# Optimization experiments

Hardware: AMD Instinct MI355X
Metric: run time of the kernel (lower is better)

The kernel has to match this reference:

```python
import jax, jax.numpy as jnp
import numpy as np
import math

B, T, C, H = 4, 2048, 768, 12
HS = C // H  # 64


def setup_inputs() -> dict:
    key = jax.random.key(0)
    ks = jax.random.split(key, 6)
    s = 1.0 / math.sqrt(C)
    return {
        "x": jax.random.normal(ks[0], (B, T, C), dtype=jnp.float32),
        "memory": jax.random.normal(ks[1], (B, T, C), dtype=jnp.float32),
        "Wq": jax.random.normal(ks[2], (C, C), dtype=jnp.float32) * s,
        "bq": jnp.zeros((C,), dtype=jnp.float32),
        "Wkv": jax.random.normal(ks[3], (C, 2 * C), dtype=jnp.float32) * s,
        "bkv": jnp.zeros((2 * C,), dtype=jnp.float32),
        "Wproj": jax.random.normal(ks[4], (C, C), dtype=jnp.float32) * s,
        "bproj": jnp.zeros((C,), dtype=jnp.float32),
    }


def reference(x, memory, Wq, bq, Wkv, bkv, Wproj, bproj):
    # q projection of decoder stream x, kv projection of encoder memory
    q = x @ Wq + bq                      # [B,T,C]
    kv = memory @ Wkv + bkv              # [B,T,2C]
    k, v = jnp.split(kv, 2, axis=2)      # [B,T,C] each

    def heads(t):
        return t.reshape(B, T, H, HS).transpose(0, 2, 1, 3)  # [B,H,T,hs]

    q, k, v = heads(q), heads(k), heads(v)
    scale = 1.0 / math.sqrt(HS)
    att = jnp.einsum("bhqd,bhkd->bhqk", q, k) * scale        # [B,H,T,T]
    att = jax.nn.softmax(att, axis=-1)
    y = jnp.einsum("bhqk,bhkd->bhqd", att, v)                # [B,H,T,hs]
    y = y.transpose(0, 2, 1, 3).reshape(B, T, C)
    return y @ Wproj + bproj
```

## Files before the change

kernel.cpp:

```cpp
#include <hip/hip_runtime.h>
#include <hip/hip_bf16.h>


#define B_  4
#define T_  2048
#define C_  768
#define H_  12
#define HS_ 64

typedef __attribute__((ext_vector_type(8))) short short8;
typedef __attribute__((ext_vector_type(4))) float f32x4;

__device__ __forceinline__ short f2bf(float f) {
    __hip_bfloat16 h = __float2bfloat16(f);
    return *reinterpret_cast<short*>(&h);
}

__device__ __forceinline__ void gload_lds16(const void* g, void* l) {
    __builtin_amdgcn_global_load_lds((const __attribute__((address_space(1))) void*)g,
                                     (__attribute__((address_space(3))) void*)l,
                                     16, 0, 0);
}


__global__ void prepass(const float* __restrict__ x, short* __restrict__ xb,
                        const float* __restrict__ mem, short* __restrict__ memb,
                        const float* __restrict__ Wq,  short* __restrict__ WqT,
                        const float* __restrict__ Wkv, short* __restrict__ WkvT,
                        const float* __restrict__ Wp,  short* __restrict__ WpT,
                        float qscale) {
    const int n4 = 8192 * 768 / 4;
    const int cvtblocks = (2 * n4) / 256;
    int bid = blockIdx.x;
    if (bid < cvtblocks) {
        int i = bid * 256 + threadIdx.x;
        const float* in; short* out;
        if (i < n4) { in = x; out = xb; }
        else        { in = mem; out = memb; i -= n4; }
        float4 v = reinterpret_cast<const float4*>(in)[i];
        short4 o;
        o.x = f2bf(v.x); o.y = f2bf(v.y); o.z = f2bf(v.z); o.w = f2bf(v.w);
        reinterpret_cast<short4*>(out)[i] = o;
        return;
    }
    __shared__ float tile[32][33];
    bid -= cvtblocks;
    const float* in; short* out; int N; float sc = 1.0f;
    if (bid < 576)       { in = Wq;  out = WqT;  N = 768;  sc = qscale; }
    else if (bid < 1728) { in = Wkv; out = WkvT; N = 1536; bid -= 576; }
    else                 { in = Wp;  out = WpT;  N = 768;  bid -= 1728; }
    const int tiles_n = N >> 5;
    const int k0 = (bid / tiles_n) * 32;
    const int n0 = (bid % tiles_n) * 32;
    const int r = threadIdx.x >> 5;
    const int c = threadIdx.x & 31;
    #pragma unroll
    for (int i = 0; i < 4; ++i)
        tile[r + 8 * i][c] = in[(size_t)(k0 + r + 8 * i) * N + n0 + c];
    __syncthreads();
    #pragma unroll
    for (int i = 0; i < 4; ++i)
        out[(size_t)(n0 + r + 8 * i) * 768 + k0 + c] = f2bf(tile[c][r + 8 * i] * sc);
}


template<int OUT_F32, int WRITE_VT>
__device__ __forceinline__ void gemm_body(const short* __restrict__ A, const short* __restrict__ BT,
                                          const float* __restrict__ bias, void* __restrict__ out,
                                          short* __restrict__ vt,
                                          int m0, int n0, int K, int ldo, float bscale,
                                          short (*As)[64], short (*Bs)[64]) {
    const int t  = threadIdx.x;
    const int wid = t >> 6;
    const int wm = wid >> 1, wn = wid & 1;
    const int lane = t & 63;
    const int lr = lane & 15;
    const int lk = (lane >> 4) * 8;

    f32x4 acc[4][4] = {};

    const int srow = wid * 32 + (lane >> 3);
    const int scol = (lane & 7) * 8;

    for (int k0 = 0; k0 < K; k0 += 64) {
        __syncthreads();
        #pragma unroll
        for (int i = 0; i < 4; ++i)
            gload_lds16(&A[(size_t)(m0 + srow + i * 8) * K + k0 + scol],
                        &As[wid * 32 + i * 8][0]);
        #pragma unroll
        for (int i = 0; i < 4; ++i)
            gload_lds16(&BT[(size_t)(n0 + srow + i * 8) * K + k0 + scol],
                        &Bs[wid * 32 + i * 8][0]);
        __syncthreads();

        #pragma unroll
        for (int ks = 0; ks < 2; ++ks) {
            const int kk = ks * 32 + lk;
            short8 a[4], b[4];
            #pragma unroll
            for (int m = 0; m < 4; ++m)
                a[m] = *reinterpret_cast<const short8*>(&As[wm*64 + m*16 + lr][kk]);
            #pragma unroll
            for (int n = 0; n < 4; ++n)
                b[n] = *reinterpret_cast<const short8*>(&Bs[wn*64 + n*16 + lr][kk]);
            #pragma unroll
            for (int m = 0; m < 4; ++m)
                #pragma unroll
                for (int n = 0; n < 4; ++n)
                    acc[m][n] = __builtin_amdgcn_mfma_f32_16x16x32_bf16(a[m], b[n], acc[m][n], 0, 0, 0);
        }
    }

    const int rb = m0 + wm * 64;
    const int cb = n0 + wn * 64;
    const int rj = (lane >> 4) * 4;
    #pragma unroll
    for (int n = 0; n < 4; ++n) {
        const int col = cb + n * 16 + lr;
        const float bv = bias[col] * bscale;
        #pragma unroll
        for (int m = 0; m < 4; ++m) {
            #pragma unroll
            for (int j = 0; j < 4; ++j) {
                const int row = rb + m * 16 + rj + j;
                const float v = acc[m][n][j] + bv;
                if (WRITE_VT && col >= 768) {
                    const int vd = col - 768;
                    const int hh = vd >> 6, dd = vd & 63;
                    const int bb = row >> 11, tt = row & 2047;
                    const int kv = tt & 63;
                    const int slot = 32 * (kv >> 5) + 8 * ((kv >> 2) & 3)
                                   + 4 * ((kv >> 4) & 1) + (kv & 3);
                    const int ptt = (tt & ~63) | slot;
                    vt[(((size_t)bb * H_ + hh) * HS_ + dd) * T_ + ptt] = f2bf(v);
                } else if (OUT_F32) {
                    reinterpret_cast<float*>(out)[(size_t)row * ldo + col] = v;
                } else {
                    reinterpret_cast<short*>(out)[(size_t)row * ldo + col] = f2bf(v);
                }
            }
        }
    }
}

__global__ void gemm_qkv(const short* __restrict__ xb,  const short* __restrict__ memb,
                         const short* __restrict__ WqT, const short* __restrict__ WkvT,
                         const float* __restrict__ bq,  const float* __restrict__ bkv,
                         short* __restrict__ qb, short* __restrict__ kvb,
                         short* __restrict__ vt, float qscale) {
    __shared__ short As[128][64];
    __shared__ short Bs[128][64];
    const int lin = blockIdx.y * 18 + blockIdx.x;
    const int swz = (lin % 8) * 144 + lin / 8;
    const int bx = swz % 18;
    const int m0 = (swz / 18) * 128;
    if (bx < 6) {
        gemm_body<0,0>(xb, WqT, bq, qb, nullptr, m0, bx * 128, 768, 768, qscale, As, Bs);
    } else {
        gemm_body<0,1>(memb, WkvT, bkv, kvb, vt, m0, (bx - 6) * 128, 768, 1536, 1.0f, As, Bs);
    }
}

__global__ void gemm_out(const short* __restrict__ yb, const short* __restrict__ WpT,
                         const float* __restrict__ bproj, float* __restrict__ out) {
    __shared__ short As[128][64];
    __shared__ short Bs[128][64];
    const int lin = blockIdx.y * 6 + blockIdx.x;
    const int swz = (lin % 8) * 48 + lin / 8;
    gemm_body<1,0>(yb, WpT, bproj, out, nullptr, (swz / 6) * 128, (swz % 6) * 128,
                   768, 768, 1.0f, As, Bs);
}


__global__ void __launch_bounds__(256)
attn_fwd14(const short* __restrict__ qb, const short* __restrict__ kvb,
           const short* __restrict__ vtb, short* __restrict__ yb) {
    __shared__ short Ks[2][64][72];
    __shared__ short Vt[2][64][72];

    const int id = blockIdx.x;
    const int pair = id % 48;
    const int b = pair / H_, h = pair % H_;
    const int q0 = (id / 48) * 128;
    const int t = threadIdx.x;
    const int w = t >> 6;
    const int lane = t & 63;
    const int lr = lane & 15;
    const int g = lane >> 4;

    const int str = t >> 2;
    const int stc = (t & 3) * 16;

    const short* Kb = kvb + (size_t)b * T_ * (2 * C_) + h * HS_;
    const short* Vb = vtb + (size_t)(b * H_ + h) * HS_ * T_;

    short8 aq[2][2];
    #pragma unroll
    for (int m = 0; m < 2; ++m)
        #pragma unroll
        for (int ks = 0; ks < 2; ++ks)
            aq[m][ks] = *reinterpret_cast<const short8*>(
                &qb[(size_t)(b * T_ + q0 + w * 32 + m * 16 + lr) * C_ + h * HS_ + ks * 32 + g * 8]);

    short8 ones8;
    #pragma unroll
    for (int i = 0; i < 8; ++i) ones8[i] = (short)0x3F80;

    f32x4 acc[2][4] = {};
    f32x4 accl[2] = {};

    uint4 kr0, kr1, vr0, vr1;
    {
        const short* gk = &Kb[(size_t)str * (2 * C_) + stc];
        const short* gv = &Vb[(size_t)str * T_ + stc];
        kr0 = *reinterpret_cast<const uint4*>(gk);
        kr1 = *reinterpret_cast<const uint4*>(gk + 8);
        vr0 = *reinterpret_cast<const uint4*>(gv);
        vr1 = *reinterpret_cast<const uint4*>(gv + 8);
    }

    int c = 0;
    for (int kv0 = 0; kv0 < T_; kv0 += 64) {
        *reinterpret_cast<uint4*>(&Ks[c][str][stc])     = kr0;
        *reinterpret_cast<uint4*>(&Ks[c][str][stc + 8]) = kr1;
        *reinterpret_cast<uint4*>(&Vt[c][str][stc])     = vr0;
        *reinterpret_cast<uint4*>(&Vt[c][str][stc + 8]) = vr1;

        if (kv0 + 64 < T_) {
            const short* gk = &Kb[(size_t)(kv0 + 64 + str) * (2 * C_) + stc];
            const short* gv = &Vb[(size_t)str * T_ + kv0 + 64 + stc];
            kr0 = *reinterpret_cast<const uint4*>(gk);
            kr1 = *reinterpret_cast<const uint4*>(gk + 8);
            vr0 = *reinterpret_cast<const uint4*>(gv);
            vr1 = *reinterpret_cast<const uint4*>(gv + 8);
        }

        __syncthreads();

        f32x4 s[2][4] = {};
        #pragma unroll
        for (int ks = 0; ks < 2; ++ks) {
            #pragma unroll
            for (int n = 0; n < 4; ++n) {
                short8 bk = *reinterpret_cast<const short8*>(&Ks[c][n * 16 + lr][ks * 32 + g * 8]);
                #pragma unroll
                for (int m = 0; m < 2; ++m)
                    s[m][n] = __builtin_amdgcn_mfma_f32_16x16x32_bf16(bk, aq[m][ks], s[m][n], 0, 0, 0);
            }
        }

        short8 pa[2][2];
        #pragma unroll
        for (int m = 0; m < 2; ++m) {
            #pragma unroll
            for (int n = 0; n < 4; ++n) {
                #pragma unroll
                for (int j = 0; j < 4; ++j)
                    s[m][n][j] = exp2f(s[m][n][j]);
            }
            #pragma unroll
            for (int ks = 0; ks < 2; ++ks) {
                pa[m][ks][0] = f2bf(s[m][2*ks][0]); pa[m][ks][1] = f2bf(s[m][2*ks][1]);
                pa[m][ks][2] = f2bf(s[m][2*ks][2]); pa[m][ks][3] = f2bf(s[m][2*ks][3]);
                pa[m][ks][4] = f2bf(s[m][2*ks+1][0]); pa[m][ks][5] = f2bf(s[m][2*ks+1][1]);
                pa[m][ks][6] = f2bf(s[m][2*ks+1][2]); pa[m][ks][7] = f2bf(s[m][2*ks+1][3]);
            }
        }

        #pragma unroll
        for (int ks = 0; ks < 2; ++ks) {
            #pragma unroll
            for (int m = 0; m < 2; ++m)
                accl[m] = __builtin_amdgcn_mfma_f32_16x16x32_bf16(pa[m][ks], ones8, accl[m], 0, 0, 0);
            #pragma unroll
            for (int n = 0; n < 4; ++n) {
                short8 bv = *reinterpret_cast<const short8*>(&Vt[c][n * 16 + lr][ks * 32 + g * 8]);
                #pragma unroll
                for (int m = 0; m < 2; ++m)
                    acc[m][n] = __builtin_amdgcn_mfma_f32_16x16x32_bf16(pa[m][ks], bv, acc[m][n], 0, 0, 0);
            }
        }

        c ^= 1;
    }

    #pragma unroll
    for (int m = 0; m < 2; ++m) {
        #pragma unroll
        for (int j = 0; j < 4; ++j) {
            const float inv = 1.f / accl[m][j];
            const size_t row = (size_t)(b * T_ + q0 + w * 32 + m * 16 + g * 4 + j);
            #pragma unroll
            for (int n = 0; n < 4; ++n)
                yb[row * C_ + h * HS_ + n * 16 + lr] = f2bf(acc[m][n][j] * inv);
        }
    }
}


extern "C" void kernel_launch(void* const* d_in, const int* in_sizes, int n_in,
                              void* d_out, int out_size, void* d_ws, size_t ws_size,
                              hipStream_t stream) {
    const float* x      = (const float*)d_in[0];
    const float* memory = (const float*)d_in[1];
    const float* Wq     = (const float*)d_in[2];
    const float* bq     = (const float*)d_in[3];
    const float* Wkv    = (const float*)d_in[4];
    const float* bkv    = (const float*)d_in[5];
    const float* Wproj  = (const float*)d_in[6];
    const float* bproj  = (const float*)d_in[7];

    char* ws = (char*)d_ws;
    size_t off = 0;
    auto alloc = [&](size_t bytes) { char* p = ws + off; off += (bytes + 255) & ~(size_t)255; return p; };
    short* xb   = (short*)alloc((size_t)8192 * 768 * 2);
    short* memb = (short*)alloc((size_t)8192 * 768 * 2);
    short* qb   = (short*)alloc((size_t)8192 * 768 * 2);
    short* kvb  = (short*)alloc((size_t)8192 * 1536 * 2);
    short* vtb  = (short*)alloc((size_t)B_ * H_ * HS_ * T_ * 2);
    short* WqT  = (short*)alloc((size_t)768 * 768 * 2);
    short* WkvT = (short*)alloc((size_t)1536 * 768 * 2);
    short* WpT  = (short*)alloc((size_t)768 * 768 * 2);

    const float qscale = 1.4426950408889634f / 8.0f;

    prepass<<<12288 + 2304, 256, 0, stream>>>(x, xb, memory, memb,
                                              Wq, WqT, Wkv, WkvT, Wproj, WpT, qscale);
    gemm_qkv<<<dim3(18, 64), 256, 0, stream>>>(xb, memb, WqT, WkvT, bq, bkv, qb, kvb, vtb, qscale);
    attn_fwd14<<<dim3(16 * 48), 256, 0, stream>>>(qb, kvb, vtb, xb );
    gemm_out<<<dim3(6, 64), 256, 0, stream>>>(xb, WpT, bproj, (float*)d_out);
}
```

Baseline: 174.1 us.

## Store K per-head contiguous with XOR swizzle and swizzle V for LDS reads

The QKV GEMM epilogue now writes K into a per-(batch,head) contiguous [T,64] buffer and XOR-swizzles the 16-byte chunks of both K and V by row. The attention kernel loads K tiles from this compact layout instead of strided rows of the interleaved KV buffer, and reads LDS fragments with the matching XOR index. The goal is contiguous global K loads and fewer LDS bank conflicts on the fragment reads. The GEMM epilogue's scattered K stores become more complex, and the LDS tiles keep their padding even though it is now redundant.

```diff
diff --git a/kernel.cpp b/kernel.cpp
--- a/kernel.cpp
+++ b/kernel.cpp
@@ -64,10 +64,10 @@
 }
 
 
-template<int OUT_F32, int WRITE_VT>
+template<int OUT_F32, int WRITE_KV>
 __device__ __forceinline__ void gemm_body(const short* __restrict__ A, const short* __restrict__ BT,
                                           const float* __restrict__ bias, void* __restrict__ out,
-                                          short* __restrict__ vt,
+                                          short* __restrict__ kt, short* __restrict__ vt,
                                           int m0, int n0, int K, int ldo, float bscale,
                                           short (*As)[64], short (*Bs)[64]) {
     const int t  = threadIdx.x;
@@ -125,15 +125,21 @@
             for (int j = 0; j < 4; ++j) {
                 const int row = rb + m * 16 + rj + j;
                 const float v = acc[m][n][j] + bv;
-                if (WRITE_VT && col >= 768) {
-                    const int vd = col - 768;
-                    const int hh = vd >> 6, dd = vd & 63;
+                if (WRITE_KV) {
                     const int bb = row >> 11, tt = row & 2047;
-                    const int kv = tt & 63;
-                    const int slot = 32 * (kv >> 5) + 8 * ((kv >> 2) & 3)
-                                   + 4 * ((kv >> 4) & 1) + (kv & 3);
-                    const int ptt = (tt & ~63) | slot;
-                    vt[(((size_t)bb * H_ + hh) * HS_ + dd) * T_ + ptt] = f2bf(v);
+                    if (col < 768) {
+                        const int hh = col >> 6, dd = col & 63;
+                        const int s = ((((dd >> 3) ^ (tt & 7)) << 3) | (dd & 7));
+                        kt[(((size_t)bb * H_ + hh) * T_ + tt) * 64 + s] = f2bf(v);
+                    } else {
+                        const int vd = col - 768;
+                        const int hh = vd >> 6, dd = vd & 63;
+                        const int kv = tt & 63;
+                        const int slot = 32 * (kv >> 5) + 8 * ((kv >> 2) & 3)
+                                       + 4 * ((kv >> 4) & 1) + (kv & 3);
+                        const int slot2 = (((slot >> 3) ^ (dd & 7)) << 3) | (slot & 7);
+                        vt[(((size_t)bb * H_ + hh) * HS_ + dd) * T_ + (tt & ~63) + slot2] = f2bf(v);
+                    }
                 } else if (OUT_F32) {
                     reinterpret_cast<float*>(out)[(size_t)row * ldo + col] = v;
                 } else {
@@ -147,7 +153,7 @@
 __global__ void gemm_qkv(const short* __restrict__ xb,  const short* __restrict__ memb,
                          const short* __restrict__ WqT, const short* __restrict__ WkvT,
                          const float* __restrict__ bq,  const float* __restrict__ bkv,
-                         short* __restrict__ qb, short* __restrict__ kvb,
+                         short* __restrict__ qb, short* __restrict__ kt,
                          short* __restrict__ vt, float qscale) {
     __shared__ short As[128][64];
     __shared__ short Bs[128][64];
@@ -156,9 +162,9 @@
     const int bx = swz % 18;
     const int m0 = (swz / 18) * 128;
     if (bx < 6) {
-        gemm_body<0,0>(xb, WqT, bq, qb, nullptr, m0, bx * 128, 768, 768, qscale, As, Bs);
+        gemm_body<0,0>(xb, WqT, bq, qb, nullptr, nullptr, m0, bx * 128, 768, 768, qscale, As, Bs);
     } else {
-        gemm_body<0,1>(memb, WkvT, bkv, kvb, vt, m0, (bx - 6) * 128, 768, 1536, 1.0f, As, Bs);
+        gemm_body<0,1>(memb, WkvT, bkv, nullptr, kt, vt, m0, (bx - 6) * 128, 768, 1536, 1.0f, As, Bs);
     }
 }
 
@@ -168,13 +174,13 @@
     __shared__ short Bs[128][64];
     const int lin = blockIdx.y * 6 + blockIdx.x;
     const int swz = (lin % 8) * 48 + lin / 8;
-    gemm_body<1,0>(yb, WpT, bproj, out, nullptr, (swz / 6) * 128, (swz % 6) * 128,
+    gemm_body<1,0>(yb, WpT, bproj, out, nullptr, nullptr, (swz / 6) * 128, (swz % 6) * 128,
                    768, 768, 1.0f, As, Bs);
 }
 
 
 __global__ void __launch_bounds__(256)
-attn_fwd14(const short* __restrict__ qb, const short* __restrict__ kvb,
+attn_fwd16(const short* __restrict__ qb, const short* __restrict__ ktb,
            const short* __restrict__ vtb, short* __restrict__ yb) {
     __shared__ short Ks[2][64][72];
     __shared__ short Vt[2][64][72];
@@ -192,7 +198,7 @@
     const int str = t >> 2;
     const int stc = (t & 3) * 16;
 
-    const short* Kb = kvb + (size_t)b * T_ * (2 * C_) + h * HS_;
+    const short* Kb = ktb + (size_t)(b * H_ + h) * T_ * 64;
     const short* Vb = vtb + (size_t)(b * H_ + h) * HS_ * T_;
 
     short8 aq[2][2];
@@ -212,7 +218,7 @@
 
     uint4 kr0, kr1, vr0, vr1;
     {
-        const short* gk = &Kb[(size_t)str * (2 * C_) + stc];
+        const short* gk = &Kb[(size_t)str * 64 + stc];
         const short* gv = &Vb[(size_t)str * T_ + stc];
         kr0 = *reinterpret_cast<const uint4*>(gk);
         kr1 = *reinterpret_cast<const uint4*>(gk + 8);
@@ -228,7 +234,7 @@
         *reinterpret_cast<uint4*>(&Vt[c][str][stc + 8]) = vr1;
 
         if (kv0 + 64 < T_) {
-            const short* gk = &Kb[(size_t)(kv0 + 64 + str) * (2 * C_) + stc];
+            const short* gk = &Kb[(size_t)(kv0 + 64 + str) * 64 + stc];
             const short* gv = &Vb[(size_t)str * T_ + kv0 + 64 + stc];
             kr0 = *reinterpret_cast<const uint4*>(gk);
             kr1 = *reinterpret_cast<const uint4*>(gk + 8);
@@ -243,7 +249,8 @@
         for (int ks = 0; ks < 2; ++ks) {
             #pragma unroll
             for (int n = 0; n < 4; ++n) {
-                short8 bk = *reinterpret_cast<const short8*>(&Ks[c][n * 16 + lr][ks * 32 + g * 8]);
+                short8 bk = *reinterpret_cast<const short8*>(
+                    &Ks[c][n * 16 + lr][(((ks * 4 + g) ^ (lr & 7)) << 3)]);
                 #pragma unroll
                 for (int m = 0; m < 2; ++m)
                     s[m][n] = __builtin_amdgcn_mfma_f32_16x16x32_bf16(bk, aq[m][ks], s[m][n], 0, 0, 0);
@@ -275,7 +282,8 @@
                 accl[m] = __builtin_amdgcn_mfma_f32_16x16x32_bf16(pa[m][ks], ones8, accl[m], 0, 0, 0);
             #pragma unroll
             for (int n = 0; n < 4; ++n) {
-                short8 bv = *reinterpret_cast<const short8*>(&Vt[c][n * 16 + lr][ks * 32 + g * 8]);
+                short8 bv = *reinterpret_cast<const short8*>(
+                    &Vt[c][n * 16 + lr][(((ks * 4 + g) ^ (lr & 7)) << 3)]);
                 #pragma unroll
                 for (int m = 0; m < 2; ++m)
                     acc[m][n] = __builtin_amdgcn_mfma_f32_16x16x32_bf16(pa[m][ks], bv, acc[m][n], 0, 0, 0);
@@ -317,7 +325,7 @@
     short* xb   = (short*)alloc((size_t)8192 * 768 * 2);
     short* memb = (short*)alloc((size_t)8192 * 768 * 2);
     short* qb   = (short*)alloc((size_t)8192 * 768 * 2);
-    short* kvb  = (short*)alloc((size_t)8192 * 1536 * 2);
+    short* ktb  = (short*)alloc((size_t)B_ * H_ * T_ * 64 * 2);
     short* vtb  = (short*)alloc((size_t)B_ * H_ * HS_ * T_ * 2);
     short* WqT  = (short*)alloc((size_t)768 * 768 * 2);
     short* WkvT = (short*)alloc((size_t)1536 * 768 * 2);
@@ -327,7 +335,7 @@
 
     prepass<<<12288 + 2304, 256, 0, stream>>>(x, xb, memory, memb,
                                               Wq, WqT, Wkv, WkvT, Wproj, WpT, qscale);
-    gemm_qkv<<<dim3(18, 64), 256, 0, stream>>>(xb, memb, WqT, WkvT, bq, bkv, qb, kvb, vtb, qscale);
-    attn_fwd14<<<dim3(16 * 48), 256, 0, stream>>>(qb, kvb, vtb, xb );
+    gemm_qkv<<<dim3(18, 64), 256, 0, stream>>>(xb, memb, WqT, WkvT, bq, bkv, qb, ktb, vtb, qscale);
+    attn_fwd16<<<dim3(16 * 48), 256, 0, stream>>>(qb, ktb, vtb, xb );
     gemm_out<<<dim3(6, 64), 256, 0, stream>>>(xb, WpT, bproj, (float*)d_out);
 }
```

New measurement: 168.7 us. 3.1% less time.
